# Kernel optimization log

Hardware: AMD Instinct MI355X
Metric: run time of the kernel (lower is better)

## Reference

```python
import jax, jax.numpy as jnp
import numpy as np

NUM_HEADS = 16
WINDOW = 512
EPS = 1e-5


def layer_norm(x, g, b):
    m = jnp.mean(x, axis=-1, keepdims=True)
    v = jnp.var(x, axis=-1, keepdims=True)
    return (x - m) * jax.lax.rsqrt(v + EPS) * g + b


def rope(x, pos):
    # x: [B,H,S,D], rotate-half RoPE with base 10000
    D = x.shape[-1]
    inv_freq = 1.0 / (10000.0 ** (jnp.arange(0, D, 2, dtype=jnp.float32) / D))
    ang = pos[:, None].astype(jnp.float32) * inv_freq  # [S, D/2]
    cos = jnp.concatenate([jnp.cos(ang), jnp.cos(ang)], axis=-1)
    sin = jnp.concatenate([jnp.sin(ang), jnp.sin(ang)], axis=-1)
    x1, x2 = jnp.split(x, 2, axis=-1)
    rot = jnp.concatenate([-x2, x1], axis=-1)
    return x * cos + rot * sin


def setup_inputs() -> dict:
    key = jax.random.key(0)
    ks = jax.random.split(key, 8)
    B, S, Dm = 2, 2048, 1024
    Dff = 4 * Dm
    sc = 0.02
    return {
        'hidden_states': jax.random.normal(ks[0], (B, S, Dm), jnp.float32),
        'ln1_g': jnp.ones((Dm,), jnp.float32),
        'ln1_b': jnp.zeros((Dm,), jnp.float32),
        'wq': jax.random.normal(ks[1], (Dm, Dm), jnp.float32) * sc,
        'bq': jnp.zeros((Dm,), jnp.float32),
        'wk': jax.random.normal(ks[2], (Dm, Dm), jnp.float32) * sc,
        'bk': jnp.zeros((Dm,), jnp.float32),
        'wv': jax.random.normal(ks[3], (Dm, Dm), jnp.float32) * sc,
        'bv': jnp.zeros((Dm,), jnp.float32),
        'wo': jax.random.normal(ks[4], (Dm, Dm), jnp.float32) * sc,
        'bo': jnp.zeros((Dm,), jnp.float32),
        'ln2_g': jnp.ones((Dm,), jnp.float32),
        'ln2_b': jnp.zeros((Dm,), jnp.float32),
        'w1': jax.random.normal(ks[5], (Dm, Dff), jnp.float32) * sc,
        'b1': jnp.zeros((Dff,), jnp.float32),
        'w2': jax.random.normal(ks[6], (Dff, Dm), jnp.float32) * sc,
        'b2': jnp.zeros((Dm,), jnp.float32),
        'global_token_indices': jax.random.randint(ks[7], (8,), 0, S, jnp.int32),
    }


def reference(hidden_states, ln1_g, ln1_b, wq, bq, wk, bk, wv, bv, wo, bo,
              ln2_g, ln2_b, w1, b1, w2, b2, global_token_indices):
    B, S, Dm = hidden_states.shape
    H = NUM_HEADS
    Dh = Dm // H

    # --- attention block ---
    x = layer_norm(hidden_states, ln1_g, ln1_b)
    heads = lambda t: t.reshape(B, S, H, Dh).transpose(0, 2, 1, 3)  # [B,H,S,Dh]
    q = heads(x @ wq + bq)
    k = heads(x @ wk + bk)
    v = heads(x @ wv + bv)

    pos = jnp.arange(S)
    q = rope(q, pos)
    k = rope(k, pos)

    scores = jnp.einsum('bhqd,bhkd->bhqk', q, k) / jnp.sqrt(jnp.float32(Dh))
    i = pos[:, None]
    j = pos[None, :]
    causal = j <= i
    band = causal & ((i - j) < WINDOW)
    is_global = jnp.zeros((S,), bool).at[global_token_indices].set(True)
    allowed = band | (causal & (is_global[None, :] | is_global[:, None]))
    scores = jnp.where(allowed[None, None], scores, jnp.float32(-1e9))
    attn = jax.nn.softmax(scores, axis=-1)
    ctx = jnp.einsum('bhqk,bhkd->bhqd', attn, v)
    ctx = ctx.transpose(0, 2, 1, 3).reshape(B, S, Dm)
    attn_out = ctx @ wo + bo
    h = hidden_states + attn_out

    # --- MLP block ---
    y = layer_norm(h, ln2_g, ln2_b)
    mlp = jax.nn.gelu(y @ w1 + b1, approximate=False) @ w2 + b2
    return h + mlp
```

## Files before the change

kernel.cpp:

```cpp
#include <hip/hip_runtime.h>

typedef unsigned short u16;
typedef __bf16 bf16x8 __attribute__((ext_vector_type(8)));
typedef short s16x8 __attribute__((ext_vector_type(8)));
typedef float f32x4 __attribute__((ext_vector_type(4)));

#define NB 2
#define SS 2048
#define DM 1024
#define NH 16
#define DH 64
#define DFF 4096

__device__ __forceinline__ u16 f2bf(float f) {
    unsigned u = __float_as_uint(f);
    u += 0x7fff + ((u >> 16) & 1);
    return (u16)(u >> 16);
}
__device__ __forceinline__ float bf2f(u16 h) {
    return __uint_as_float(((unsigned)h) << 16);
}
__device__ __forceinline__ void gld_lds16(const void* g, void* l) {
    __builtin_amdgcn_global_load_lds(
        (const __attribute__((address_space(1))) unsigned int*)(size_t)g,
        (__attribute__((address_space(3))) unsigned int*)(unsigned)(size_t)l,
        16, 0, 0);
}
__device__ __forceinline__ float gelu_f(float x) {
    return 0.5f * x * (1.f + erff(x * 0.70710678118654752f));
}

__global__ void wtrans_kernel(const float* __restrict__ w, u16* __restrict__ wt,
                              int K, int N) {
    __shared__ unsigned tl[64][65];
    int n0 = blockIdx.x * 64, k0 = blockIdx.y * 64, t = threadIdx.x;
    for (int it = 0; it < 16; ++it) {
        int e = it * 256 + t; int r = e >> 6, c = e & 63;
        tl[r][c] = f2bf(w[(size_t)(k0 + r) * N + n0 + c]);
    }
    __syncthreads();
    for (int it = 0; it < 16; ++it) {
        int e = it * 256 + t; int r = e >> 6, c = e & 63;
        wt[(size_t)(n0 + r) * K + k0 + c] = (u16)tl[c][r];
    }
}

__global__ void wtrans4_kernel(const float* __restrict__ a, const float* __restrict__ b,
                               const float* __restrict__ c, const float* __restrict__ d,
                               u16* __restrict__ oa, u16* __restrict__ ob,
                               u16* __restrict__ oc, u16* __restrict__ od) {
    __shared__ unsigned tl[64][65];
    const float* w; u16* wt;
    switch (blockIdx.z) {
        case 0: w = a; wt = oa; break;
        case 1: w = b; wt = ob; break;
        case 2: w = c; wt = oc; break;
        default: w = d; wt = od; break;
    }
    int n0 = blockIdx.x * 64, k0 = blockIdx.y * 64, t = threadIdx.x;
    for (int it = 0; it < 16; ++it) {
        int e = it * 256 + t; int r = e >> 6, cc = e & 63;
        tl[r][cc] = f2bf(w[(size_t)(k0 + r) * DM + n0 + cc]);
    }
    __syncthreads();
    for (int it = 0; it < 16; ++it) {
        int e = it * 256 + t; int r = e >> 6, cc = e & 63;
        wt[(size_t)(n0 + r) * DM + k0 + cc] = (u16)tl[cc][r];
    }
}

__global__ void build_aux(const int* __restrict__ gti, unsigned long long* __restrict__ kmask,
                          const float* __restrict__ bq, const float* __restrict__ bk,
                          const float* __restrict__ bv, float* __restrict__ bias3) {
    int t = threadIdx.x;
    if (t < 32) {
        unsigned long long m = 0ull;
        #pragma unroll
        for (int i = 0; i < 8; ++i) {
            int g = gti[i];
            if ((g >> 6) == t) m |= 1ull << (g & 63);
        }
        kmask[t] = m;
    }
    for (int i = t; i < 1024; i += 256) {
        bias3[i] = bq[i]; bias3[1024 + i] = bk[i]; bias3[2048 + i] = bv[i];
    }
}

template <bool INIT>
__global__ __launch_bounds__(256) void ln_kernel(const float* __restrict__ x,
                                                 const float* __restrict__ g,
                                                 const float* __restrict__ b,
                                                 u16* __restrict__ out,
                                                 const float* __restrict__ ib,
                                                 float* __restrict__ iout) {
    int row = blockIdx.x, t = threadIdx.x;
    const float4 v = ((const float4*)(x + (size_t)row * DM))[t];
    float s  = v.x + v.y + v.z + v.w;
    float sq = v.x * v.x + v.y * v.y + v.z * v.z + v.w * v.w;
    #pragma unroll
    for (int m = 1; m < 64; m <<= 1) { s += __shfl_xor(s, m); sq += __shfl_xor(sq, m); }
    __shared__ float ss[4], ssq[4];
    int wv = t >> 6, lane = t & 63;
    if (lane == 0) { ss[wv] = s; ssq[wv] = sq; }
    __syncthreads();
    s  = ss[0] + ss[1] + ss[2] + ss[3];
    sq = ssq[0] + ssq[1] + ssq[2] + ssq[3];
    float mean = s * (1.f / DM);
    float var  = sq * (1.f / DM) - mean * mean;
    float rs   = rsqrtf(var + 1e-5f);
    float4 gg = ((const float4*)g)[t];
    float4 bb = ((const float4*)b)[t];
    ushort4 o;
    o.x = f2bf((v.x - mean) * rs * gg.x + bb.x);
    o.y = f2bf((v.y - mean) * rs * gg.y + bb.y);
    o.z = f2bf((v.z - mean) * rs * gg.z + bb.z);
    o.w = f2bf((v.w - mean) * rs * gg.w + bb.w);
    ((ushort4*)(out + (size_t)row * DM))[t] = o;
    if (INIT) {
        float4 b2 = ((const float4*)ib)[t];
        float4 iv; iv.x = v.x + b2.x; iv.y = v.y + b2.y; iv.z = v.z + b2.z; iv.w = v.w + b2.w;
        ((float4*)(iout + (size_t)row * DM))[t] = iv;
    }
}

__global__ __launch_bounds__(256) void rope_kernel(const u16* __restrict__ qkv,
                                                   u16* __restrict__ qh,
                                                   u16* __restrict__ kh) {
    int idx = blockIdx.x * 256 + threadIdx.x;
    int d = idx & 31;
    int s = (idx >> 5) & (SS - 1);
    int h = (idx >> 16) & (NH - 1);
    int b = idx >> 20;
    size_t src = ((size_t)(b * SS + s)) * 3072 + h * DH + d;
    size_t dst = ((size_t)((b * NH + h) * SS + s)) * DH + d;
    float inv = powf(10000.f, -(float)d * (1.f / 32.f));
    float ang = (float)s * inv;
    float sn, cs;
    sincosf(ang, &sn, &cs);
    const float QSC = 0.125f;
    float x1 = bf2f(qkv[src]), x2 = bf2f(qkv[src + 32]);
    qh[dst]      = f2bf((x1 * cs - x2 * sn) * QSC);
    qh[dst + 32] = f2bf((x2 * cs + x1 * sn) * QSC);
    x1 = bf2f(qkv[src + 1024]); x2 = bf2f(qkv[src + 1024 + 32]);
    kh[dst]      = f2bf(x1 * cs - x2 * sn);
    kh[dst + 32] = f2bf(x2 * cs + x1 * sn);
}

__global__ __launch_bounds__(256) void vtrans_kernel(const u16* __restrict__ qkv,
                                                     u16* __restrict__ vt) {
    __shared__ unsigned tile[64][65];
    int st = blockIdx.x, bh = blockIdx.y;
    int b = bh >> 4, h = bh & 15, t = threadIdx.x;
    const u16* src = qkv + ((size_t)b * SS + st * 64) * 3072 + 2048 + h * DH;
    for (int it = 0; it < 16; ++it) {
        int e = it * 256 + t; int r = e >> 6, c = e & 63;
        tile[r][c] = src[(size_t)r * 3072 + c];
    }
    __syncthreads();
    u16* dst = vt + ((size_t)bh * DH) * SS + st * 64;
    for (int it = 0; it < 16; ++it) {
        int e = it * 256 + t; int d = e >> 6, s = e & 63;
        dst[(size_t)d * SS + s] = (u16)tile[s][d];
    }
}

template <int MODE>
__global__ __launch_bounds__(256) void gemm_bt(const u16* __restrict__ A,
                                               const u16* __restrict__ Bt,
                                               const float* __restrict__ bias,
                                               const float* __restrict__ res,
                                               void* __restrict__ Cout,
                                               int M, int N, int K, int ldk) {
    const int bm = blockIdx.y * 128, bn = blockIdx.x * 128;
    const int koff = blockIdx.z * K;
    const int t = threadIdx.x, wv = t >> 6, lane = t & 63;
    const int lr = lane & 15, lq = lane >> 4;
    const int wm = (wv >> 1) * 64, wn = (wv & 1) * 64;
    __shared__ __align__(16) u16 As[2][128 * 64];
    __shared__ __align__(16) u16 Bs[2][128 * 64];
    f32x4 acc[4][4] = {};

    auto stage = [&](int kb, int buf) {
        #pragma unroll
        for (int p = 0; p < 4; ++p) {
            int c = p * 256 + t;
            int r = c >> 3;
            int gc = ((c & 7) ^ (r & 7)) * 8;
            gld_lds16(A + (size_t)(bm + r) * ldk + kb + gc,
                      As[buf] + (size_t)(p * 256 + wv * 64) * 8);
            gld_lds16(Bt + (size_t)(bn + r) * ldk + kb + gc,
                      Bs[buf] + (size_t)(p * 256 + wv * 64) * 8);
        }
    };

    stage(koff, 0);
    int pb = 0;
    for (int k0 = 0; k0 < K; k0 += 64) {
        __syncthreads();
        if (k0 + 64 < K) stage(koff + k0 + 64, pb ^ 1);
        const u16* Ac = As[pb];
        const u16* Bc = Bs[pb];
        #pragma unroll
        for (int ks = 0; ks < 2; ++ks) {
            bf16x8 af[4], bfr[4];
            #pragma unroll
            for (int mi = 0; mi < 4; ++mi) {
                int row = wm + mi * 16 + lr;
                af[mi] = *(const bf16x8*)&Ac[row * 64 + (((ks * 4 + lq) ^ (row & 7)) * 8)];
            }
            #pragma unroll
            for (int ni = 0; ni < 4; ++ni) {
                int row = wn + ni * 16 + lr;
                bfr[ni] = *(const bf16x8*)&Bc[row * 64 + (((ks * 4 + lq) ^ (row & 7)) * 8)];
            }
            #pragma unroll
            for (int mi = 0; mi < 4; ++mi)
                #pragma unroll
                for (int ni = 0; ni < 4; ++ni)
                    acc[mi][ni] = __builtin_amdgcn_mfma_f32_16x16x32_bf16(af[mi], bfr[ni], acc[mi][ni], 0, 0, 0);
        }
        pb ^= 1;
    }
    #pragma unroll
    for (int mi = 0; mi < 4; ++mi) {
        int row0 = bm + wm + mi * 16 + lq * 4;
        #pragma unroll
        for (int ni = 0; ni < 4; ++ni) {
            int col = bn + wn + ni * 16 + lr;
            float bv = (MODE == 3) ? 0.f : bias[col];
            #pragma unroll
            for (int r = 0; r < 4; ++r) {
                float v = acc[mi][ni][r] + bv;
                size_t off = (size_t)(row0 + r) * N + col;
                if (MODE == 1) v += res[off];
                if (MODE == 2) v = gelu_f(v);
                if (MODE == 0 || MODE == 2) ((u16*)Cout)[off] = f2bf(v);
                else if (MODE == 1)         ((float*)Cout)[off] = v;
                else                        atomicAdd((float*)Cout + off, v);
            }
        }
    }
}

template <int MODE>
__global__ __launch_bounds__(512, 2) void gemm256(const u16* __restrict__ A,
                                                  const u16* __restrict__ Bt,
                                                  const float* __restrict__ bias,
                                                  void* __restrict__ Cout,
                                                  int M, int N, int K, int ldk) {
    const int bm = blockIdx.y * 256, bn = blockIdx.x * 256;
    const int koff = blockIdx.z * K;
    const int t = threadIdx.x, wv = t >> 6, lane = t & 63;
    const int lr = lane & 15, lq = lane >> 4;
    const int wm = (wv >> 2) * 128, wn = (wv & 3) * 64;
    __shared__ __align__(16) u16 As[4 * 256 * 32];
    __shared__ __align__(16) u16 Bs[4 * 256 * 32];
    f32x4 acc[8][4] = {};

    auto stage = [&](int st) {
        const int buf = st & 3;
        const int kb = koff + st * 32;
        #pragma unroll
        for (int p = 0; p < 2; ++p) {
            int c = p * 512 + t;
            int r = c >> 2, sl = c & 3;
            int gc = (sl ^ ((r >> 1) & 3)) * 8;
            gld_lds16(A + (size_t)(bm + r) * ldk + kb + gc,
                      As + (size_t)buf * 8192 + (size_t)(p * 512 + wv * 64) * 8);
            gld_lds16(Bt + (size_t)(bn + r) * ldk + kb + gc,
                      Bs + (size_t)buf * 8192 + (size_t)(p * 512 + wv * 64) * 8);
        }
    };

    auto compute = [&](int s) {
        const u16* Ac = As + (size_t)(s & 3) * 8192;
        const u16* Bc = Bs + (size_t)(s & 3) * 8192;
        bf16x8 af[8], bfv[4];
        #pragma unroll
        for (int mi = 0; mi < 8; ++mi) {
            int row = wm + mi * 16 + lr;
            af[mi] = *(const bf16x8*)&Ac[row * 32 + ((lq ^ ((row >> 1) & 3)) * 8)];
        }
        #pragma unroll
        for (int ni = 0; ni < 4; ++ni) {
            int row = wn + ni * 16 + lr;
            bfv[ni] = *(const bf16x8*)&Bc[row * 32 + ((lq ^ ((row >> 1) & 3)) * 8)];
        }
        __builtin_amdgcn_s_setprio(1);
        #pragma unroll
        for (int mi = 0; mi < 8; ++mi)
            #pragma unroll
            for (int ni = 0; ni < 4; ++ni)
                acc[mi][ni] = __builtin_amdgcn_mfma_f32_16x16x32_bf16(af[mi], bfv[ni], acc[mi][ni], 0, 0, 0);
        __builtin_amdgcn_s_setprio(0);
    };

    const int NS = K >> 5;
    stage(0);
    stage(1);
    for (int s = 0; s < NS - 2; ++s) {
        stage(s + 2);
        asm volatile("s_waitcnt vmcnt(8) lgkmcnt(0)" ::: "memory");
        __builtin_amdgcn_s_barrier();
        asm volatile("" ::: "memory");
        compute(s);
    }
    asm volatile("s_waitcnt vmcnt(4) lgkmcnt(0)" ::: "memory");
    __builtin_amdgcn_s_barrier();
    asm volatile("" ::: "memory");
    compute(NS - 2);
    asm volatile("s_waitcnt vmcnt(0) lgkmcnt(0)" ::: "memory");
    __builtin_amdgcn_s_barrier();
    asm volatile("" ::: "memory");
    compute(NS - 1);

    #pragma unroll
    for (int mi = 0; mi < 8; ++mi) {
        int row0 = bm + wm + mi * 16 + lq * 4;
        #pragma unroll
        for (int ni = 0; ni < 4; ++ni) {
            int col = bn + wn + ni * 16 + lr;
            float bv = (MODE == 3) ? 0.f : bias[col];
            #pragma unroll
            for (int r = 0; r < 4; ++r) {
                float v = acc[mi][ni][r] + bv;
                size_t off = (size_t)(row0 + r) * N + col;
                if (MODE == 2) v = gelu_f(v);
                if (MODE == 0 || MODE == 2) ((u16*)Cout)[off] = f2bf(v);
                else                        atomicAdd((float*)Cout + off, v);
            }
        }
    }
}

__global__ __launch_bounds__(256) void attn_kernel(const u16* __restrict__ qh,
                                                   const u16* __restrict__ kh,
                                                   const u16* __restrict__ vt,
                                                   const unsigned long long* __restrict__ kmask,
                                                   u16* __restrict__ ctx) {
    const int qt = blockIdx.x, bh = blockIdx.y;
    const int b = bh >> 4, h = bh & 15;
    const int t = threadIdx.x, wv = t >> 6, lane = t & 63;
    const int lr = lane & 15, lq = lane >> 4;
    const int q0 = qt * 64;

    __shared__ __align__(16) u16 Qs[64 * 64];
    __shared__ __align__(16) u16 Ks[2][64 * 64];
    __shared__ __align__(16) u16 Vs[2][64 * 64];
    __shared__ __align__(16) u16 Ps[64 * 64];

    const u16* qbase = qh + ((size_t)bh * SS) * DH;
    const u16* kbase = kh + ((size_t)bh * SS) * DH;
    const u16* vbase = vt + ((size_t)bh * DH) * SS;

    #pragma unroll
    for (int p = 0; p < 2; ++p) {
        int c = p * 256 + t; int r = c >> 3, sl = c & 7;
        gld_lds16(qbase + (size_t)(q0 + r) * DH + ((sl ^ (r & 7)) * 8),
                  Qs + (size_t)(p * 256 + wv * 64) * 8);
    }

    float sum_part[4] = {0.f, 0.f, 0.f, 0.f};
    f32x4 acc_o[4] = {};

    const int lim = qt - 8;
    int cur = 0;
    while (cur < lim && kmask[cur] == 0ull) ++cur;
    {
        int k0 = cur * 64;
        #pragma unroll
        for (int p = 0; p < 2; ++p) {
            int c = p * 256 + t; int r = c >> 3; int gc = ((c & 7) ^ (r & 7)) * 8;
            gld_lds16(kbase + (size_t)(k0 + r) * DH + gc, Ks[0] + (size_t)(p * 256 + wv * 64) * 8);
            gld_lds16(vbase + (size_t)r * SS + k0 + gc,  Vs[0] + (size_t)(p * 256 + wv * 64) * 8);
        }
    }
    int pb = 0;
    while (cur >= 0) {
        int nxt = cur + 1;
        while (nxt < lim && kmask[nxt] == 0ull) ++nxt;
        if (nxt > qt) nxt = -1;
        __syncthreads();
        if (nxt >= 0) {
            int k0n = nxt * 64;
            #pragma unroll
            for (int p = 0; p < 2; ++p) {
                int c = p * 256 + t; int r = c >> 3; int gc = ((c & 7) ^ (r & 7)) * 8;
                gld_lds16(kbase + (size_t)(k0n + r) * DH + gc, Ks[pb ^ 1] + (size_t)(p * 256 + wv * 64) * 8);
                gld_lds16(vbase + (size_t)r * SS + k0n + gc,  Vs[pb ^ 1] + (size_t)(p * 256 + wv * 64) * 8);
            }
        }
        const u16* Kt = Ks[pb];
        const u16* Vt = Vs[pb];
        const int k0 = cur * 64;

        f32x4 s_acc[4] = {};
        #pragma unroll
        for (int ks = 0; ks < 2; ++ks) {
            const int arow = wv * 16 + lr;
            bf16x8 af = *(const bf16x8*)&Qs[arow * 64 + (((ks * 4 + lq) ^ (arow & 7)) * 8)];
            #pragma unroll
            for (int ni = 0; ni < 4; ++ni) {
                const int brow = ni * 16 + lr;
                bf16x8 bfr = *(const bf16x8*)&Kt[brow * 64 + (((ks * 4 + lq) ^ (brow & 7)) * 8)];
                s_acc[ni] = __builtin_amdgcn_mfma_f32_16x16x32_bf16(af, bfr, s_acc[ni], 0, 0, 0);
            }
        }
        float sv[4][4];
        if (cur >= qt - 7 && cur != qt) {
            #pragma unroll
            for (int ni = 0; ni < 4; ++ni)
                #pragma unroll
                for (int r = 0; r < 4; ++r) sv[ni][r] = __expf(s_acc[ni][r]);
        } else if (cur == qt) {
            #pragma unroll
            for (int ni = 0; ni < 4; ++ni) {
                int j = ni * 16 + lr;
                #pragma unroll
                for (int r = 0; r < 4; ++r) {
                    int i = wv * 16 + lq * 4 + r;
                    float p = __expf(s_acc[ni][r]);
                    sv[ni][r] = (j <= i) ? p : 0.f;
                }
            }
        } else {
            unsigned long long cm = kmask[cur];
            #pragma unroll
            for (int ni = 0; ni < 4; ++ni) {
                int j = k0 + ni * 16 + lr;
                bool gj = (cm >> (ni * 16 + lr)) & 1ull;
                #pragma unroll
                for (int r = 0; r < 4; ++r) {
                    int i = q0 + wv * 16 + lq * 4 + r;
                    bool ok = ((i - j) < 512) | gj;
                    float p = __expf(s_acc[ni][r]);
                    sv[ni][r] = ok ? p : 0.f;
                }
            }
        }
        #pragma unroll
        for (int ni = 0; ni < 4; ++ni) {
            int col = ni * 16 + lr;
            #pragma unroll
            for (int r = 0; r < 4; ++r) {
                int row = wv * 16 + lq * 4 + r;
                sum_part[r] += sv[ni][r];
                Ps[row * 64 + (((col >> 3) ^ (row & 7)) * 8) + (col & 7)] = f2bf(sv[ni][r]);
            }
        }
        #pragma unroll
        for (int ks = 0; ks < 2; ++ks) {
            const int arow = wv * 16 + lr;
            bf16x8 af = *(const bf16x8*)&Ps[arow * 64 + (((ks * 4 + lq) ^ (arow & 7)) * 8)];
            #pragma unroll
            for (int ni = 0; ni < 4; ++ni) {
                const int brow = ni * 16 + lr;
                bf16x8 bfr = *(const bf16x8*)&Vt[brow * 64 + (((ks * 4 + lq) ^ (brow & 7)) * 8)];
                acc_o[ni] = __builtin_amdgcn_mfma_f32_16x16x32_bf16(af, bfr, acc_o[ni], 0, 0, 0);
            }
        }
        cur = nxt; pb ^= 1;
    }
    float inv_l[4];
    #pragma unroll
    for (int r = 0; r < 4; ++r) {
        float ls = sum_part[r];
        #pragma unroll
        for (int m = 1; m < 16; m <<= 1) ls += __shfl_xor(ls, m, 16);
        inv_l[r] = 1.f / ls;
    }
    u16* obase = ctx + ((size_t)b * SS) * DM + h * DH;
    #pragma unroll
    for (int ni = 0; ni < 4; ++ni)
        #pragma unroll
        for (int r = 0; r < 4; ++r) {
            int i = q0 + wv * 16 + lq * 4 + r;
            obase[(size_t)i * DM + ni * 16 + lr] = f2bf(acc_o[ni][r] * inv_l[r]);
        }
}

__global__ __launch_bounds__(256) void attn_fix_kernel(const u16* __restrict__ qh,
                                                       const u16* __restrict__ kh,
                                                       const u16* __restrict__ qkv,
                                                       const int* __restrict__ gti,
                                                       u16* __restrict__ ctx) {
    const int gidx = blockIdx.x, bh = blockIdx.y;
    const int b = bh >> 4, h = bh & 15;
    const int t = threadIdx.x, wv = t >> 6, lane = t & 63;
    const int i = gti[gidx];

    __shared__ float qsh[64];
    if (t < 64) qsh[t] = bf2f(qh[((size_t)bh * SS + i) * DH + t]);
    __syncthreads();
    float qreg[64];
    #pragma unroll
    for (int c = 0; c < 16; ++c) {
        float4 qv = ((const float4*)qsh)[c];
        qreg[c * 4 + 0] = qv.x; qreg[c * 4 + 1] = qv.y;
        qreg[c * 4 + 2] = qv.z; qreg[c * 4 + 3] = qv.w;
    }

    const u16* kb = kh + (size_t)bh * SS * DH;
    const u16* vb = qkv + (size_t)b * SS * 3072 + 2048 + h * DH;

    float Oacc[64];
    #pragma unroll
    for (int d = 0; d < 64; ++d) Oacc[d] = 0.f;
    float lacc = 0.f;

    for (int j0 = wv * 64; j0 <= i; j0 += 256) {
        const int j = j0 + lane;
        const bool valid = (j <= i);
        const int jc = valid ? j : i;
        const s16x8* krow = (const s16x8*)(kb + (size_t)jc * DH);
        float part[8];
        #pragma unroll
        for (int c = 0; c < 8; ++c) {
            s16x8 kv = krow[c];
            float p0 = 0.f;
            #pragma unroll
            for (int e = 0; e < 8; ++e) p0 += qreg[c * 8 + e] * bf2f((u16)kv[e]);
            part[c] = p0;
        }
        float s = ((part[0] + part[1]) + (part[2] + part[3])) +
                  ((part[4] + part[5]) + (part[6] + part[7]));
        const float p = valid ? __expf(s) : 0.f;
        lacc += p;
        const s16x8* vrow = (const s16x8*)(vb + (size_t)jc * 3072);
        #pragma unroll
        for (int c = 0; c < 8; ++c) {
            s16x8 vv = vrow[c];
            #pragma unroll
            for (int e = 0; e < 8; ++e) Oacc[c * 8 + e] += p * bf2f((u16)vv[e]);
        }
    }
    #pragma unroll
    for (int m = 1; m < 64; m <<= 1) {
        lacc += __shfl_xor(lacc, m);
        #pragma unroll
        for (int d = 0; d < 64; ++d) Oacc[d] += __shfl_xor(Oacc[d], m);
    }
    float out = 0.f;
    #pragma unroll
    for (int d = 0; d < 64; ++d) out = (lane == d) ? Oacc[d] : out;
    __shared__ float osum[4][64];
    __shared__ float lsum[4];
    osum[wv][lane] = out;
    if (lane == 0) lsum[wv] = lacc;
    __syncthreads();
    if (wv == 0) {
        float ot = osum[0][lane] + osum[1][lane] + osum[2][lane] + osum[3][lane];
        float lt = lsum[0] + lsum[1] + lsum[2] + lsum[3];
        ctx[((size_t)b * SS + i) * DM + h * DH + lane] = f2bf(ot / lt);
    }
}

extern "C" void kernel_launch(void* const* d_in, const int* in_sizes, int n_in,
                              void* d_out, int out_size, void* d_ws, size_t ws_size,
                              hipStream_t stream) {
    (void)in_sizes; (void)n_in; (void)out_size; (void)ws_size;
    const float* hidden = (const float*)d_in[0];
    const float* ln1_g  = (const float*)d_in[1];
    const float* ln1_b  = (const float*)d_in[2];
    const float* wq = (const float*)d_in[3];  const float* bq = (const float*)d_in[4];
    const float* wk = (const float*)d_in[5];  const float* bk = (const float*)d_in[6];
    const float* wv = (const float*)d_in[7];  const float* bv = (const float*)d_in[8];
    const float* wo = (const float*)d_in[9];  const float* bo = (const float*)d_in[10];
    const float* ln2_g = (const float*)d_in[11];
    const float* ln2_b = (const float*)d_in[12];
    const float* w1 = (const float*)d_in[13]; const float* b1 = (const float*)d_in[14];
    const float* w2 = (const float*)d_in[15]; const float* b2 = (const float*)d_in[16];
    const int*  gti = (const int*)d_in[17];

    char* ws = (char*)d_ws;
    const size_t MB = 1u << 20;
    u16* wqt  = (u16*)(ws + 0 * MB);
    u16* wkt  = (u16*)(ws + 2 * MB);
    u16* wvt  = (u16*)(ws + 4 * MB);
    u16* wot  = (u16*)(ws + 6 * MB);
    u16* w1t  = (u16*)(ws + 8 * MB);
    u16* w2t  = (u16*)(ws + 16 * MB);
    u16* xb   = (u16*)(ws + 24 * MB);
    u16* ctx  = xb;
    u16* qkv  = (u16*)(ws + 32 * MB);
    u16* qhb  = (u16*)(ws + 56 * MB);
    u16* khb  = (u16*)(ws + 64 * MB);
    u16* vtb  = (u16*)(ws + 72 * MB);
    float* hb = (float*)(ws + 80 * MB);
    u16* act  = (u16*)(ws + 32 * MB);
    u16* yb   = (u16*)(ws + 64 * MB);
    unsigned long long* kmask = (unsigned long long*)(ws + 96 * MB);
    float* bias3 = (float*)(ws + 96 * MB + 8192);

    wtrans4_kernel<<<dim3(16, 16, 4), 256, 0, stream>>>(wq, wk, wv, wo, wqt, wkt, wvt, wot);
    wtrans_kernel<<<dim3(64, 16), 256, 0, stream>>>(w1, w1t, DM, DFF);
    wtrans_kernel<<<dim3(16, 64), 256, 0, stream>>>(w2, w2t, DFF, DM);
    build_aux<<<1, 256, 0, stream>>>(gti, kmask, bq, bk, bv, bias3);

    ln_kernel<false><<<NB * SS, 256, 0, stream>>>(hidden, ln1_g, ln1_b, xb, nullptr, nullptr);

    gemm256<0><<<dim3(3072 / 256, (NB * SS) / 256), 512, 0, stream>>>(
        xb, wqt, bias3, qkv, NB * SS, 3072, DM, DM);

    rope_kernel<<<(NB * NH * SS * 32) / 256, 256, 0, stream>>>(qkv, qhb, khb);
    vtrans_kernel<<<dim3(SS / 64, NB * NH), 256, 0, stream>>>(qkv, vtb);

    attn_kernel<<<dim3(SS / 64, NB * NH), 256, 0, stream>>>(qhb, khb, vtb, kmask, ctx);
    attn_fix_kernel<<<dim3(8, NB * NH), 256, 0, stream>>>(qhb, khb, qkv, gti, ctx);

    gemm_bt<1><<<dim3(8, 32), 256, 0, stream>>>(ctx, wot, bo, hidden, hb, NB * SS, DM, DM, DM);
    ln_kernel<true><<<NB * SS, 256, 0, stream>>>(hb, ln2_g, ln2_b, yb, b2, (float*)d_out);
    gemm256<2><<<dim3(DFF / 256, (NB * SS) / 256), 512, 0, stream>>>(
        yb, w1t, b1, act, NB * SS, DFF, DM, DM);
    gemm256<3><<<dim3(DM / 256, (NB * SS) / 256, 4), 512, 0, stream>>>(
        act, w2t, nullptr, d_out, NB * SS, DM, DFF / 4, DFF);
}
```

Measured before the change: 419.5 us.

## Restructure 256-tile GEMM into quadrant-interleaved pipeline and move W2 GEMM to gemm_bt

Rewrites the 256x256 GEMM main loop to use 64-wide K tiles double-buffered in two halves per operand. It interleaves global-to-LDS staging with four quadrant MFMA phases separated by barriers, so loads overlap compute. The split-K atomic path is dropped from gemm256, and the second MLP GEMM now runs through the smaller gemm_bt kernel with split-K of 2 instead of 4. The extra barriers add sync overhead, and the different tiling changes occupancy for the W2 GEMM.

```diff
diff --git a/kernel.cpp b/kernel.cpp
--- a/kernel.cpp
+++ b/kernel.cpp
@@ -212,7 +212,7 @@
             #pragma unroll
             for (int ni = 0; ni < 4; ++ni) {
                 int row = wn + ni * 16 + lr;
-                bfr[ni] = *(const bf16x8*)&Bc[row * 64 + (((ks * 4 + lq) ^ (row & 7)) * 8)];
+                bfr[ni] = *(const bf16x8*)&Bs[pb][row * 64 + (((ks * 4 + lq) ^ (row & 7)) * 8)];
             }
             #pragma unroll
             for (int mi = 0; mi < 4; ++mi)
@@ -250,70 +250,129 @@
                                                   void* __restrict__ Cout,
                                                   int M, int N, int K, int ldk) {
     const int bm = blockIdx.y * 256, bn = blockIdx.x * 256;
-    const int koff = blockIdx.z * K;
     const int t = threadIdx.x, wv = t >> 6, lane = t & 63;
     const int lr = lane & 15, lq = lane >> 4;
     const int wm = (wv >> 2) * 128, wn = (wv & 3) * 64;
-    __shared__ __align__(16) u16 As[4 * 256 * 32];
-    __shared__ __align__(16) u16 Bs[4 * 256 * 32];
+    const int awb = (wv >> 2) * 64;
+    const int bwb = (wv & 3) * 32;
+    __shared__ __align__(16) u16 As[2 * 2 * 128 * 64];
+    __shared__ __align__(16) u16 Bs[2 * 2 * 128 * 64];
     f32x4 acc[8][4] = {};
-
-    auto stage = [&](int st) {
-        const int buf = st & 3;
-        const int kb = koff + st * 32;
+    bf16x8 aA[4][2], bA[2][2], bB[2][2];
+
+    const u16 *pAsrc[2][2], *pBsrc[2][2];
+    #pragma unroll
+    for (int g = 0; g < 2; ++g)
         #pragma unroll
         for (int p = 0; p < 2; ++p) {
             int c = p * 512 + t;
-            int r = c >> 2, sl = c & 3;
-            int gc = (sl ^ ((r >> 1) & 3)) * 8;
-            gld_lds16(A + (size_t)(bm + r) * ldk + kb + gc,
-                      As + (size_t)buf * 8192 + (size_t)(p * 512 + wv * 64) * 8);
-            gld_lds16(Bt + (size_t)(bn + r) * ldk + kb + gc,
-                      Bs + (size_t)buf * 8192 + (size_t)(p * 512 + wv * 64) * 8);
-        }
+            int glr = c >> 3, sl = c & 7;
+            int sc = (sl ^ (glr & 7)) * 8;
+            int grA = (glr & 63) + g * 64 + ((glr >> 6) << 7);
+            int grB = (glr & 31) + g * 32 + ((glr >> 5) << 6);
+            pAsrc[g][p] = A  + (size_t)(bm + grA) * ldk + sc;
+            pBsrc[g][p] = Bt + (size_t)(bn + grB) * ldk + sc;
+        }
+    auto AsP = [&](int db, int g) { return As + (size_t)(db * 2 + g) * 8192; };
+    auto BsP = [&](int db, int g) { return Bs + (size_t)(db * 2 + g) * 8192; };
+    auto stA = [&](int g, int db, int ku) {
+        #pragma unroll
+        for (int p = 0; p < 2; ++p)
+            gld_lds16(pAsrc[g][p] + ku, AsP(db, g) + (size_t)(p * 512 + wv * 64) * 8);
     };
-
-    auto compute = [&](int s) {
-        const u16* Ac = As + (size_t)(s & 3) * 8192;
-        const u16* Bc = Bs + (size_t)(s & 3) * 8192;
-        bf16x8 af[8], bfv[4];
-        #pragma unroll
-        for (int mi = 0; mi < 8; ++mi) {
-            int row = wm + mi * 16 + lr;
-            af[mi] = *(const bf16x8*)&Ac[row * 32 + ((lq ^ ((row >> 1) & 3)) * 8)];
-        }
-        #pragma unroll
-        for (int ni = 0; ni < 4; ++ni) {
-            int row = wn + ni * 16 + lr;
-            bfv[ni] = *(const bf16x8*)&Bc[row * 32 + ((lq ^ ((row >> 1) & 3)) * 8)];
-        }
+    auto stB = [&](int g, int db, int ku) {
+        #pragma unroll
+        for (int p = 0; p < 2; ++p)
+            gld_lds16(pBsrc[g][p] + ku, BsP(db, g) + (size_t)(p * 512 + wv * 64) * 8);
+    };
+    auto loadA = [&](const u16* base) {
+        #pragma unroll
+        for (int mi2 = 0; mi2 < 4; ++mi2)
+            #pragma unroll
+            for (int ks = 0; ks < 2; ++ks) {
+                int glr = awb + mi2 * 16 + lr;
+                aA[mi2][ks] = *(const bf16x8*)&base[glr * 64 + (((ks * 4 + lq) ^ (glr & 7)) * 8)];
+            }
+    };
+    auto loadB = [&](const u16* base, bf16x8 (&dst)[2][2]) {
+        #pragma unroll
+        for (int ni2 = 0; ni2 < 2; ++ni2)
+            #pragma unroll
+            for (int ks = 0; ks < 2; ++ks) {
+                int glr = bwb + ni2 * 16 + lr;
+                dst[ni2][ks] = *(const bf16x8*)&base[glr * 64 + (((ks * 4 + lq) ^ (glr & 7)) * 8)];
+            }
+    };
+    auto mmac = [&](int qm, int qn, bf16x8 (&bb)[2][2]) {
         __builtin_amdgcn_s_setprio(1);
         #pragma unroll
-        for (int mi = 0; mi < 8; ++mi)
-            #pragma unroll
-            for (int ni = 0; ni < 4; ++ni)
-                acc[mi][ni] = __builtin_amdgcn_mfma_f32_16x16x32_bf16(af[mi], bfv[ni], acc[mi][ni], 0, 0, 0);
+        for (int mi2 = 0; mi2 < 4; ++mi2)
+            #pragma unroll
+            for (int ni2 = 0; ni2 < 2; ++ni2)
+                #pragma unroll
+                for (int ks = 0; ks < 2; ++ks)
+                    acc[qm * 4 + mi2][qn * 2 + ni2] =
+                        __builtin_amdgcn_mfma_f32_16x16x32_bf16(
+                            aA[mi2][ks], bb[ni2][ks], acc[qm * 4 + mi2][qn * 2 + ni2], 0, 0, 0);
         __builtin_amdgcn_s_setprio(0);
     };
-
-    const int NS = K >> 5;
-    stage(0);
-    stage(1);
-    for (int s = 0; s < NS - 2; ++s) {
-        stage(s + 2);
-        asm volatile("s_waitcnt vmcnt(8) lgkmcnt(0)" ::: "memory");
-        __builtin_amdgcn_s_barrier();
-        asm volatile("" ::: "memory");
-        compute(s);
-    }
-    asm volatile("s_waitcnt vmcnt(4) lgkmcnt(0)" ::: "memory");
+    #define LGKM0_FENCE  do { asm volatile("s_waitcnt lgkmcnt(0)" ::: "memory"); \
+                              __builtin_amdgcn_sched_barrier(0); } while (0)
+
+    const int NT = K >> 6;
+    stA(0, 0, 0); stA(1, 0, 0); stB(0, 0, 0); stB(1, 0, 0);
+    asm volatile("s_waitcnt vmcnt(2)" ::: "memory");
     __builtin_amdgcn_s_barrier();
-    asm volatile("" ::: "memory");
-    compute(NS - 2);
-    asm volatile("s_waitcnt vmcnt(0) lgkmcnt(0)" ::: "memory");
-    __builtin_amdgcn_s_barrier();
-    asm volatile("" ::: "memory");
-    compute(NS - 1);
+
+    for (int kt = 0; kt < NT - 1; ++kt) {
+        const int db = kt & 1, nb2 = db ^ 1;
+        const int ku = (kt + 1) * 64;
+        loadA(AsP(db, 0)); loadB(BsP(db, 0), bA);
+        stA(0, nb2, ku);
+        __builtin_amdgcn_s_barrier();
+        LGKM0_FENCE;
+        mmac(0, 0, bA);
+        asm volatile("s_waitcnt vmcnt(2)" ::: "memory");
+        __builtin_amdgcn_s_barrier();
+        loadB(BsP(db, 1), bB);
+        stA(1, nb2, ku);
+        __builtin_amdgcn_s_barrier();
+        LGKM0_FENCE;
+        mmac(0, 1, bB);
+        __builtin_amdgcn_s_barrier();
+        loadA(AsP(db, 1));
+        stB(0, nb2, ku);
+        __builtin_amdgcn_s_barrier();
+        LGKM0_FENCE;
+        mmac(1, 1, bB);
+        __builtin_amdgcn_s_barrier();
+        stB(1, nb2, ku);
+        __builtin_amdgcn_s_barrier();
+        LGKM0_FENCE;
+        mmac(1, 0, bA);
+        asm volatile("s_waitcnt vmcnt(2)" ::: "memory");
+        __builtin_amdgcn_s_barrier();
+    }
+    {
+        const int db = (NT - 1) & 1;
+        loadA(AsP(db, 0)); loadB(BsP(db, 0), bA);
+        __builtin_amdgcn_s_barrier();
+        LGKM0_FENCE;
+        mmac(0, 0, bA);
+        asm volatile("s_waitcnt vmcnt(0)" ::: "memory");
+        __builtin_amdgcn_s_barrier();
+        loadB(BsP(db, 1), bB);
+        __builtin_amdgcn_s_barrier();
+        LGKM0_FENCE;
+        mmac(0, 1, bB);
+        __builtin_amdgcn_s_barrier();
+        loadA(AsP(db, 1));
+        __builtin_amdgcn_s_barrier();
+        LGKM0_FENCE;
+        mmac(1, 1, bB);
+        mmac(1, 0, bA);
+    }
+    #undef LGKM0_FENCE
 
     #pragma unroll
     for (int mi = 0; mi < 8; ++mi) {
@@ -321,14 +380,13 @@
         #pragma unroll
         for (int ni = 0; ni < 4; ++ni) {
             int col = bn + wn + ni * 16 + lr;
-            float bv = (MODE == 3) ? 0.f : bias[col];
+            float bv = bias[col];
             #pragma unroll
             for (int r = 0; r < 4; ++r) {
                 float v = acc[mi][ni][r] + bv;
                 size_t off = (size_t)(row0 + r) * N + col;
                 if (MODE == 2) v = gelu_f(v);
-                if (MODE == 0 || MODE == 2) ((u16*)Cout)[off] = f2bf(v);
-                else                        atomicAdd((float*)Cout + off, v);
+                ((u16*)Cout)[off] = f2bf(v);
             }
         }
     }
@@ -613,6 +671,5 @@
     ln_kernel<true><<<NB * SS, 256, 0, stream>>>(hb, ln2_g, ln2_b, yb, b2, (float*)d_out);
     gemm256<2><<<dim3(DFF / 256, (NB * SS) / 256), 512, 0, stream>>>(
         yb, w1t, b1, act, NB * SS, DFF, DM, DM);
-    gemm256<3><<<dim3(DM / 256, (NB * SS) / 256, 4), 512, 0, stream>>>(
-        act, w2t, nullptr, d_out, NB * SS, DM, DFF / 4, DFF);
-}
+    gemm_bt<3><<<dim3(8, 32, 2), 256, 0, stream>>>(act, w2t, nullptr, nullptr, d_out, NB * SS, DM, DFF / 2, DFF);
+}
```

Result: faster. 397.1 us (-5.3%).
